# Kernel tuning notes

Hardware: AMD Instinct MI355X
Metric: run time of the kernel (lower is better)

## Reference

```python
import jax, jax.numpy as jnp
import numpy as np

IN_DIM, OUT_DIM, HIDDEN = 64, 64, 128


def _cell(x, h, c, w_ih, w_hh, b_ih, b_hh):
    # PyTorch LSTM gate order: i, f, g, o
    gates = x @ w_ih.T + b_ih + h @ w_hh.T + b_hh
    i, f, g, o = jnp.split(gates, 4, axis=-1)
    c = jax.nn.sigmoid(f) * c + jax.nn.sigmoid(i) * jnp.tanh(g)
    h = jax.nn.sigmoid(o) * jnp.tanh(c)
    return h, c


def setup_inputs() -> dict:
    key = jax.random.key(0)
    ks = jax.random.split(key, 12)
    B, S = 8192, 128
    s = 1.0 / np.sqrt(HIDDEN)
    u = lambda k, shp: jax.random.uniform(k, shp, jnp.float32, -s, s)
    return {
        "x": jax.random.normal(ks[0], (B, S, IN_DIM), jnp.float32),
        "w_ih0": u(ks[1], (4 * HIDDEN, IN_DIM)),
        "w_hh0": u(ks[2], (4 * HIDDEN, HIDDEN)),
        "b_ih0": u(ks[3], (4 * HIDDEN,)),
        "b_hh0": u(ks[4], (4 * HIDDEN,)),
        "w_ih1": u(ks[5], (4 * HIDDEN, HIDDEN)),
        "w_hh1": u(ks[6], (4 * HIDDEN, HIDDEN)),
        "b_ih1": u(ks[7], (4 * HIDDEN,)),
        "b_hh1": u(ks[8], (4 * HIDDEN,)),
        "w_dec": u(ks[9], (OUT_DIM, HIDDEN)),
        "b_dec": u(ks[10], (OUT_DIM,)),
        "pred_steps": 20,
    }


def reference(x, w_ih0, w_hh0, b_ih0, b_hh0, w_ih1, w_hh1, b_ih1, b_hh1, w_dec, b_dec, pred_steps):
    B = x.shape[0]
    z = jnp.zeros((B, HIDDEN), x.dtype)

    def enc_step(carry, xt):
        h0, c0, h1, c1 = carry
        h0, c0 = _cell(xt, h0, c0, w_ih0, w_hh0, b_ih0, b_hh0)
        h1, c1 = _cell(h0, h1, c1, w_ih1, w_hh1, b_ih1, b_hh1)
        return (h0, c0, h1, c1), None

    carry, _ = jax.lax.scan(enc_step, (z, z, z, z), jnp.swapaxes(x, 0, 1))

    def dec_step(carry, _):
        inp, h0, c0, h1, c1 = carry
        h0, c0 = _cell(inp, h0, c0, w_ih0, w_hh0, b_ih0, b_hh0)
        h1, c1 = _cell(h0, h1, c1, w_ih1, w_hh1, b_ih1, b_hh1)
        p = h1 @ w_dec.T + b_dec
        return (p, h0, c0, h1, c1), p

    _, preds = jax.lax.scan(dec_step, (x[:, -1, :],) + carry, None, length=pred_steps)
    return jnp.swapaxes(preds, 0, 1)  # [B, pred_steps, out_dim]
```

## Files before the change

kernel.cpp:

```cpp
#include <hip/hip_runtime.h>
#include <cstdint>
#include <cstddef>

#define BATCH  8192
#define INDIM  64
#define OUTDIM 64
#define HID    128
#define BT     32
#define NT     512
#define KP     328
#define COLH0  64
#define COLH1  192
#define KB0    6
#define KB1    8
#define KBD    4

#define W0U    0
#define W1U    196608
#define WDU    458752
#define B0F    237568
#define B1F    238080
#define BDF    238592
#define NPACK  238656

typedef unsigned short u16;
typedef __attribute__((ext_vector_type(8))) short bfrag;
typedef __attribute__((ext_vector_type(4))) float facc;

__device__ __forceinline__ u16 f2bf(float x) {
  uint32_t u = __float_as_uint(x);
  return (u16)((u + 0x7fffu + ((u >> 16) & 1u)) >> 16);
}
__device__ __forceinline__ float bf2f(u16 h) {
  return __uint_as_float(((uint32_t)h) << 16);
}
__device__ __forceinline__ float fsig(float x) { return 1.0f / (1.0f + __expf(-x)); }
__device__ __forceinline__ float ftanh(float x) {
  float e = __expf(2.0f * x);
  return 1.0f - 2.0f / (e + 1.0f);
}
__device__ __forceinline__ facc splat4(float v) {
  facc a; a[0] = v; a[1] = v; a[2] = v; a[3] = v; return a;
}

template <int KB>
__device__ __forceinline__ void gemm_block(const u16* __restrict__ wt,
                                           const u16 (&Hhi)[BT][KP],
                                           const u16 (&Hlo)[BT][KP],
                                           int colOff, int c, int g, int ntq,
                                           facc (&acc)[2][4]) {
#pragma unroll
  for (int kb = 0; kb < KB; ++kb) {
    bfrag bh[4], bl[4], ah[2], al[2];
#pragma unroll
    for (int t = 0; t < 4; ++t) {
      const u16* p = wt + (((ntq + t) * KB + kb) * 2) * 512;
      bh[t] = *(const bfrag*)p;
      bl[t] = *(const bfrag*)(p + 512);
    }
    const int k0 = colOff + kb * 32 + g * 8;
#pragma unroll
    for (int mt = 0; mt < 2; ++mt) {
      ah[mt] = *(const bfrag*)&Hhi[mt * 16 + c][k0];
      al[mt] = *(const bfrag*)&Hlo[mt * 16 + c][k0];
    }
#pragma unroll
    for (int mt = 0; mt < 2; ++mt)
#pragma unroll
      for (int t = 0; t < 4; ++t) {
        facc a = acc[mt][t];
        a = __builtin_amdgcn_mfma_f32_16x16x32_bf16(ah[mt], bh[t], a, 0, 0, 0);
        a = __builtin_amdgcn_mfma_f32_16x16x32_bf16(ah[mt], bl[t], a, 0, 0, 0);
        a = __builtin_amdgcn_mfma_f32_16x16x32_bf16(al[mt], bh[t], a, 0, 0, 0);
        acc[mt][t] = a;
      }
  }
}

__global__ __launch_bounds__(NT, 2) void lstm_kernel(
    const float* __restrict__ x, const void* __restrict__ pkv,
    float* __restrict__ out, int S, int P) {
  __shared__ __align__(16) u16 Ahi[BT][KP];
  __shared__ __align__(16) u16 Alo[BT][KP];

  const u16* pku = (const u16*)pkv;
  const float* pkf = (const float*)pkv;

  const int tid = threadIdx.x;
  const int lane = tid & 63;
  const int w = tid >> 6;
  const int c = lane & 15;
  const int g = lane >> 4;
  const int b0 = blockIdx.x * BT;

  for (int i = tid; i < BT * KP; i += NT) {
    (&Ahi[0][0])[i] = 0;
    (&Alo[0][0])[i] = 0;
  }

  float b0r[4], b1r[4];
#pragma unroll
  for (int t = 0; t < 4; ++t) {
    b0r[t] = pkf[B0F + (w * 4 + t) * 16 + c];
    b1r[t] = pkf[B1F + (w * 4 + t) * 16 + c];
  }
  const int ntd = w & 3, mtd = w >> 2;
  const float bdr = pkf[BDF + ntd * 16 + c];

  float c0r[8], c1r[8];
#pragma unroll
  for (int q = 0; q < 8; ++q) { c0r[q] = 0.f; c1r[q] = 0.f; }

  const u16* w0t = pku + W0U + lane * 8;
  const u16* w1t = pku + W1U + lane * 8;
  const u16* wdt = pku + WDU + lane * 8;

  __syncthreads();

  const int T = S + P;
  for (int step = 0; step < T; ++step) {
    if (step < S) {
      const int s = tid >> 4, c4 = (tid & 15) * 4;
      const float4 v = *(const float4*)(x + ((size_t)(b0 + s) * S + step) * INDIM + c4);
      float vv[4] = {v.x, v.y, v.z, v.w};
      u16 h4[4], l4[4];
#pragma unroll
      for (int q = 0; q < 4; ++q) {
        h4[q] = f2bf(vv[q]);
        l4[q] = f2bf(vv[q] - bf2f(h4[q]));
      }
      uint2 hp, lp;
      hp.x = (uint32_t)h4[0] | ((uint32_t)h4[1] << 16);
      hp.y = (uint32_t)h4[2] | ((uint32_t)h4[3] << 16);
      lp.x = (uint32_t)l4[0] | ((uint32_t)l4[1] << 16);
      lp.y = (uint32_t)l4[2] | ((uint32_t)l4[3] << 16);
      *(uint2*)&Ahi[s][c4] = hp;
      *(uint2*)&Alo[s][c4] = lp;
    }
    __syncthreads();

    facc acc[2][4];
#pragma unroll
    for (int mt = 0; mt < 2; ++mt)
#pragma unroll
      for (int t = 0; t < 4; ++t) acc[mt][t] = splat4(b0r[t]);
    gemm_block<KB0>(w0t, Ahi, Alo, 0, c, g, w * 4, acc);
    __syncthreads();
#pragma unroll
    for (int mt = 0; mt < 2; ++mt)
#pragma unroll
      for (int r = 0; r < 4; ++r) {
        float gi = fsig(acc[mt][0][r]);
        float gf = fsig(acc[mt][1][r]);
        float gg = ftanh(acc[mt][2][r]);
        float go = fsig(acc[mt][3][r]);
        float cn = fmaf(gf, c0r[mt * 4 + r], gi * gg);
        c0r[mt * 4 + r] = cn;
        float hv = go * ftanh(cn);
        const int s = mt * 16 + g * 4 + r;
        u16 hh = f2bf(hv);
        Ahi[s][COLH0 + w * 16 + c] = hh;
        Alo[s][COLH0 + w * 16 + c] = f2bf(hv - bf2f(hh));
      }
    __syncthreads();

#pragma unroll
    for (int mt = 0; mt < 2; ++mt)
#pragma unroll
      for (int t = 0; t < 4; ++t) acc[mt][t] = splat4(b1r[t]);
    gemm_block<KB1>(w1t, Ahi, Alo, COLH0, c, g, w * 4, acc);
    __syncthreads();
#pragma unroll
    for (int mt = 0; mt < 2; ++mt)
#pragma unroll
      for (int r = 0; r < 4; ++r) {
        float gi = fsig(acc[mt][0][r]);
        float gf = fsig(acc[mt][1][r]);
        float gg = ftanh(acc[mt][2][r]);
        float go = fsig(acc[mt][3][r]);
        float cn = fmaf(gf, c1r[mt * 4 + r], gi * gg);
        c1r[mt * 4 + r] = cn;
        float hv = go * ftanh(cn);
        const int s = mt * 16 + g * 4 + r;
        u16 hh = f2bf(hv);
        Ahi[s][COLH1 + w * 16 + c] = hh;
        Alo[s][COLH1 + w * 16 + c] = f2bf(hv - bf2f(hh));
      }

    if (step >= S) {
      __syncthreads();
      facc da = splat4(bdr);
#pragma unroll
      for (int kb = 0; kb < KBD; ++kb) {
        const u16* p = wdt + ((ntd * KBD + kb) * 2) * 512;
        bfrag wbh = *(const bfrag*)p;
        bfrag wbl = *(const bfrag*)(p + 512);
        const int k0 = COLH1 + kb * 32 + g * 8;
        bfrag dah = *(const bfrag*)&Ahi[mtd * 16 + c][k0];
        bfrag dal = *(const bfrag*)&Alo[mtd * 16 + c][k0];
        da = __builtin_amdgcn_mfma_f32_16x16x32_bf16(dah, wbh, da, 0, 0, 0);
        da = __builtin_amdgcn_mfma_f32_16x16x32_bf16(dah, wbl, da, 0, 0, 0);
        da = __builtin_amdgcn_mfma_f32_16x16x32_bf16(dal, wbh, da, 0, 0, 0);
      }
      const int dstep = step - S;
#pragma unroll
      for (int r = 0; r < 4; ++r) {
        const int s = mtd * 16 + g * 4 + r;
        const int o = ntd * 16 + c;
        float pv = da[r];
        out[((size_t)(b0 + s) * P + dstep) * OUTDIM + o] = pv;
        u16 hh = f2bf(pv);
        Ahi[s][o] = hh;
        Alo[s][o] = f2bf(pv - bf2f(hh));
      }
    }
  }
}

__global__ void prepack_kernel(const float* __restrict__ wih0, const float* __restrict__ whh0,
                               const float* __restrict__ bih0, const float* __restrict__ bhh0,
                               const float* __restrict__ wih1, const float* __restrict__ whh1,
                               const float* __restrict__ bih1, const float* __restrict__ bhh1,
                               const float* __restrict__ wdec, const float* __restrict__ bdec,
                               void* __restrict__ pko) {
  int idx = blockIdx.x * blockDim.x + threadIdx.x;
  if (idx >= NPACK) return;
  u16* pu = (u16*)pko;
  float* pf = (float*)pko;
  if (idx < 98304) {
    int nt = idx / 3072, rem = idx % 3072;
    int kb = rem >> 9, q = rem & 511, ln = q >> 3, j = q & 7;
    int n = nt * 16 + (ln & 15);
    int row = ((n >> 4) & 3) * HID + (n >> 6) * 16 + (n & 15);
    int k = kb * 32 + (ln >> 4) * 8 + j;
    float wv = (k < INDIM) ? wih0[row * INDIM + k] : whh0[row * HID + k - INDIM];
    u16 hi = f2bf(wv), lo = f2bf(wv - bf2f(hi));
    int base = W0U + ((nt * KB0 + kb) * 2) * 512;
    pu[base + q] = hi;
    pu[base + 512 + q] = lo;
  } else if (idx < 229376) {
    int r = idx - 98304;
    int nt = r >> 12, rem = r & 4095;
    int kb = rem >> 9, q = rem & 511, ln = q >> 3, j = q & 7;
    int n = nt * 16 + (ln & 15);
    int row = ((n >> 4) & 3) * HID + (n >> 6) * 16 + (n & 15);
    int k = kb * 32 + (ln >> 4) * 8 + j;
    float wv = (k < HID) ? wih1[row * HID + k] : whh1[row * HID + k - HID];
    u16 hi = f2bf(wv), lo = f2bf(wv - bf2f(hi));
    int base = W1U + ((nt * KB1 + kb) * 2) * 512;
    pu[base + q] = hi;
    pu[base + 512 + q] = lo;
  } else if (idx < 237568) {
    int r = idx - 229376;
    int nt = r >> 11, rem = r & 2047;
    int kb = rem >> 9, q = rem & 511, ln = q >> 3, j = q & 7;
    int o = nt * 16 + (ln & 15);
    int k = kb * 32 + (ln >> 4) * 8 + j;
    float wv = wdec[o * HID + k];
    u16 hi = f2bf(wv), lo = f2bf(wv - bf2f(hi));
    int base = WDU + ((nt * KBD + kb) * 2) * 512;
    pu[base + q] = hi;
    pu[base + 512 + q] = lo;
  } else if (idx < 238080) {
    int n = idx - 237568;
    int row = ((n >> 4) & 3) * HID + (n >> 6) * 16 + (n & 15);
    pf[B0F + n] = bih0[row] + bhh0[row];
  } else if (idx < 238592) {
    int n = idx - 238080;
    int row = ((n >> 4) & 3) * HID + (n >> 6) * 16 + (n & 15);
    pf[B1F + n] = bih1[row] + bhh1[row];
  } else {
    int o = idx - 238592;
    pf[BDF + o] = bdec[o];
  }
}

extern "C" void kernel_launch(void* const* d_in, const int* in_sizes, int n_in,
                              void* d_out, int out_size, void* d_ws, size_t ws_size,
                              hipStream_t stream) {
  const float* x    = (const float*)d_in[0];
  const float* wih0 = (const float*)d_in[1];
  const float* whh0 = (const float*)d_in[2];
  const float* bih0 = (const float*)d_in[3];
  const float* bhh0 = (const float*)d_in[4];
  const float* wih1 = (const float*)d_in[5];
  const float* whh1 = (const float*)d_in[6];
  const float* bih1 = (const float*)d_in[7];
  const float* bhh1 = (const float*)d_in[8];
  const float* wdec = (const float*)d_in[9];
  const float* bdec = (const float*)d_in[10];
  float* out = (float*)d_out;

  const int S = in_sizes[0] / (BATCH * INDIM);
  const int P = out_size / (BATCH * OUTDIM);

  prepack_kernel<<<(NPACK + 255) / 256, 256, 0, stream>>>(
      wih0, whh0, bih0, bhh0, wih1, whh1, bih1, bhh1, wdec, bdec, d_ws);

  lstm_kernel<<<BATCH / BT, NT, 0, stream>>>(x, d_ws, out, S, P);
}
```

Measured before the change: 4.720 ms.

## Double batch tile to 64 rows and prefetch weight fragments across k-blocks

Each block now handles 64 batch rows instead of 32, so every weight fragment read from global memory feeds twice as many MFMAs, and the grid shrinks to half as many blocks. The GEMM loop also double-buffers weight fragments, loading the next k-block while the current one is in use. The cost is roughly double LDS (about 84 KB per block) and many more accumulator and cell-state registers, which will likely drop occupancy below the two blocks per CU that launch_bounds requests. The prefetch buffers add further register pressure and risk spills.

```diff
diff --git a/kernel.cpp b/kernel.cpp
--- a/kernel.cpp
+++ b/kernel.cpp
@@ -6,7 +6,7 @@
 #define INDIM  64
 #define OUTDIM 64
 #define HID    128
-#define BT     32
+#define BT     64
 #define NT     512
 #define KP     328
 #define COLH0  64
@@ -48,30 +48,41 @@
                                            const u16 (&Hhi)[BT][KP],
                                            const u16 (&Hlo)[BT][KP],
                                            int colOff, int c, int g, int ntq,
-                                           facc (&acc)[2][4]) {
+                                           facc (&acc)[4][4]) {
+  bfrag wa[8], wb[8];
+#pragma unroll
+  for (int t = 0; t < 4; ++t) {
+    const u16* p = wt + (((ntq + t) * KB + 0) * 2) * 512;
+    wa[t * 2]     = *(const bfrag*)p;
+    wa[t * 2 + 1] = *(const bfrag*)(p + 512);
+  }
 #pragma unroll
   for (int kb = 0; kb < KB; ++kb) {
-    bfrag bh[4], bl[4], ah[2], al[2];
-#pragma unroll
-    for (int t = 0; t < 4; ++t) {
-      const u16* p = wt + (((ntq + t) * KB + kb) * 2) * 512;
-      bh[t] = *(const bfrag*)p;
-      bl[t] = *(const bfrag*)(p + 512);
+    bfrag (&cur)[8] = (kb & 1) ? wb : wa;
+    bfrag (&nxt)[8] = (kb & 1) ? wa : wb;
+    if (kb + 1 < KB) {
+#pragma unroll
+      for (int t = 0; t < 4; ++t) {
+        const u16* p = wt + (((ntq + t) * KB + kb + 1) * 2) * 512;
+        nxt[t * 2]     = *(const bfrag*)p;
+        nxt[t * 2 + 1] = *(const bfrag*)(p + 512);
+      }
     }
     const int k0 = colOff + kb * 32 + g * 8;
-#pragma unroll
-    for (int mt = 0; mt < 2; ++mt) {
+    bfrag ah[4], al[4];
+#pragma unroll
+    for (int mt = 0; mt < 4; ++mt) {
       ah[mt] = *(const bfrag*)&Hhi[mt * 16 + c][k0];
       al[mt] = *(const bfrag*)&Hlo[mt * 16 + c][k0];
     }
 #pragma unroll
-    for (int mt = 0; mt < 2; ++mt)
+    for (int mt = 0; mt < 4; ++mt)
 #pragma unroll
       for (int t = 0; t < 4; ++t) {
         facc a = acc[mt][t];
-        a = __builtin_amdgcn_mfma_f32_16x16x32_bf16(ah[mt], bh[t], a, 0, 0, 0);
-        a = __builtin_amdgcn_mfma_f32_16x16x32_bf16(ah[mt], bl[t], a, 0, 0, 0);
-        a = __builtin_amdgcn_mfma_f32_16x16x32_bf16(al[mt], bh[t], a, 0, 0, 0);
+        a = __builtin_amdgcn_mfma_f32_16x16x32_bf16(ah[mt], cur[t * 2],     a, 0, 0, 0);
+        a = __builtin_amdgcn_mfma_f32_16x16x32_bf16(ah[mt], cur[t * 2 + 1], a, 0, 0, 0);
+        a = __builtin_amdgcn_mfma_f32_16x16x32_bf16(al[mt], cur[t * 2],     a, 0, 0, 0);
         acc[mt][t] = a;
       }
   }
@@ -107,9 +118,9 @@
   const int ntd = w & 3, mtd = w >> 2;
   const float bdr = pkf[BDF + ntd * 16 + c];
 
-  float c0r[8], c1r[8];
-#pragma unroll
-  for (int q = 0; q < 8; ++q) { c0r[q] = 0.f; c1r[q] = 0.f; }
+  float c0r[16], c1r[16];
+#pragma unroll
+  for (int q = 0; q < 16; ++q) { c0r[q] = 0.f; c1r[q] = 0.f; }
 
   const u16* w0t = pku + W0U + lane * 8;
   const u16* w1t = pku + W1U + lane * 8;
@@ -120,34 +131,38 @@
   const int T = S + P;
   for (int step = 0; step < T; ++step) {
     if (step < S) {
-      const int s = tid >> 4, c4 = (tid & 15) * 4;
-      const float4 v = *(const float4*)(x + ((size_t)(b0 + s) * S + step) * INDIM + c4);
-      float vv[4] = {v.x, v.y, v.z, v.w};
-      u16 h4[4], l4[4];
-#pragma unroll
-      for (int q = 0; q < 4; ++q) {
-        h4[q] = f2bf(vv[q]);
-        l4[q] = f2bf(vv[q] - bf2f(h4[q]));
-      }
-      uint2 hp, lp;
-      hp.x = (uint32_t)h4[0] | ((uint32_t)h4[1] << 16);
-      hp.y = (uint32_t)h4[2] | ((uint32_t)h4[3] << 16);
-      lp.x = (uint32_t)l4[0] | ((uint32_t)l4[1] << 16);
-      lp.y = (uint32_t)l4[2] | ((uint32_t)l4[3] << 16);
-      *(uint2*)&Ahi[s][c4] = hp;
-      *(uint2*)&Alo[s][c4] = lp;
+#pragma unroll
+      for (int i = 0; i < 2; ++i) {
+        const int q = tid + NT * i;
+        const int s = q >> 4, c4 = (q & 15) * 4;
+        const float4 v = *(const float4*)(x + ((size_t)(b0 + s) * S + step) * INDIM + c4);
+        float vv[4] = {v.x, v.y, v.z, v.w};
+        u16 h4[4], l4[4];
+#pragma unroll
+        for (int qq = 0; qq < 4; ++qq) {
+          h4[qq] = f2bf(vv[qq]);
+          l4[qq] = f2bf(vv[qq] - bf2f(h4[qq]));
+        }
+        uint2 hp, lp;
+        hp.x = (uint32_t)h4[0] | ((uint32_t)h4[1] << 16);
+        hp.y = (uint32_t)h4[2] | ((uint32_t)h4[3] << 16);
+        lp.x = (uint32_t)l4[0] | ((uint32_t)l4[1] << 16);
+        lp.y = (uint32_t)l4[2] | ((uint32_t)l4[3] << 16);
+        *(uint2*)&Ahi[s][c4] = hp;
+        *(uint2*)&Alo[s][c4] = lp;
+      }
     }
     __syncthreads();
 
-    facc acc[2][4];
-#pragma unroll
-    for (int mt = 0; mt < 2; ++mt)
+    facc acc[4][4];
+#pragma unroll
+    for (int mt = 0; mt < 4; ++mt)
 #pragma unroll
       for (int t = 0; t < 4; ++t) acc[mt][t] = splat4(b0r[t]);
     gemm_block<KB0>(w0t, Ahi, Alo, 0, c, g, w * 4, acc);
     __syncthreads();
 #pragma unroll
-    for (int mt = 0; mt < 2; ++mt)
+    for (int mt = 0; mt < 4; ++mt)
 #pragma unroll
       for (int r = 0; r < 4; ++r) {
         float gi = fsig(acc[mt][0][r]);
@@ -165,13 +180,13 @@
     __syncthreads();
 
 #pragma unroll
-    for (int mt = 0; mt < 2; ++mt)
+    for (int mt = 0; mt < 4; ++mt)
 #pragma unroll
       for (int t = 0; t < 4; ++t) acc[mt][t] = splat4(b1r[t]);
     gemm_block<KB1>(w1t, Ahi, Alo, COLH0, c, g, w * 4, acc);
     __syncthreads();
 #pragma unroll
-    for (int mt = 0; mt < 2; ++mt)
+    for (int mt = 0; mt < 4; ++mt)
 #pragma unroll
       for (int r = 0; r < 4; ++r) {
         float gi = fsig(acc[mt][0][r]);
@@ -189,29 +204,37 @@
 
     if (step >= S) {
       __syncthreads();
-      facc da = splat4(bdr);
+      facc da[2] = {splat4(bdr), splat4(bdr)};
 #pragma unroll
       for (int kb = 0; kb < KBD; ++kb) {
         const u16* p = wdt + ((ntd * KBD + kb) * 2) * 512;
         bfrag wbh = *(const bfrag*)p;
         bfrag wbl = *(const bfrag*)(p + 512);
         const int k0 = COLH1 + kb * 32 + g * 8;
-        bfrag dah = *(const bfrag*)&Ahi[mtd * 16 + c][k0];
-        bfrag dal = *(const bfrag*)&Alo[mtd * 16 + c][k0];
-        da = __builtin_amdgcn_mfma_f32_16x16x32_bf16(dah, wbh, da, 0, 0, 0);
-        da = __builtin_amdgcn_mfma_f32_16x16x32_bf16(dah, wbl, da, 0, 0, 0);
-        da = __builtin_amdgcn_mfma_f32_16x16x32_bf16(dal, wbh, da, 0, 0, 0);
+#pragma unroll
+        for (int mi = 0; mi < 2; ++mi) {
+          const int mt = mtd + mi * 2;
+          bfrag dah = *(const bfrag*)&Ahi[mt * 16 + c][k0];
+          bfrag dal = *(const bfrag*)&Alo[mt * 16 + c][k0];
+          da[mi] = __builtin_amdgcn_mfma_f32_16x16x32_bf16(dah, wbh, da[mi], 0, 0, 0);
+          da[mi] = __builtin_amdgcn_mfma_f32_16x16x32_bf16(dah, wbl, da[mi], 0, 0, 0);
+          da[mi] = __builtin_amdgcn_mfma_f32_16x16x32_bf16(dal, wbh, da[mi], 0, 0, 0);
+        }
       }
       const int dstep = step - S;
 #pragma unroll
-      for (int r = 0; r < 4; ++r) {
-        const int s = mtd * 16 + g * 4 + r;
-        const int o = ntd * 16 + c;
-        float pv = da[r];
-        out[((size_t)(b0 + s) * P + dstep) * OUTDIM + o] = pv;
-        u16 hh = f2bf(pv);
-        Ahi[s][o] = hh;
-        Alo[s][o] = f2bf(pv - bf2f(hh));
+      for (int mi = 0; mi < 2; ++mi) {
+        const int mt = mtd + mi * 2;
+#pragma unroll
+        for (int r = 0; r < 4; ++r) {
+          const int s = mt * 16 + g * 4 + r;
+          const int o = ntd * 16 + c;
+          float pv = da[mi][r];
+          out[((size_t)(b0 + s) * P + dstep) * OUTDIM + o] = pv;
+          u16 hh = f2bf(pv);
+          Ahi[s][o] = hh;
+          Alo[s][o] = f2bf(pv - bf2f(hh));
+        }
       }
     }
   }
```

New measurement: 5.508 ms. 1.17x slower.

## Double-buffer hidden state, split M across 16 waves, prefetch x, trim barriers

Applied to the files above, without the earlier changes.

Moves the block to 1024 threads, with each wave handling half the batch rows instead of both M tiles. It double-buffers the h0/h1 columns in LDS by step parity, which removes the write-after-read barriers between the GEMM and the activation phases. The next timestep's x is prefetched into registers and written during the layer-0 epilogue. Lighter lgkmcnt-only barriers and s_setprio around the MFMA bursts are added. The cost is one block per CU with a larger LDS footprint, and each wave now reloads the full weight fragments while doing half the M work, which doubles weight traffic per step.

```diff
diff --git a/kernel.cpp b/kernel.cpp
--- a/kernel.cpp
+++ b/kernel.cpp
@@ -7,13 +7,14 @@
 #define OUTDIM 64
 #define HID    128
 #define BT     32
-#define NT     512
-#define KP     328
-#define COLH0  64
-#define COLH1  192
+#define NT     1024
+#define KP2    584
 #define KB0    6
 #define KB1    8
 #define KBD    4
+
+#define XH0(p) (64 + 128 * (p))
+#define XH1(p) (320 + 128 * (p))
 
 #define W0U    0
 #define W1U    196608
@@ -43,45 +44,51 @@
   facc a; a[0] = v; a[1] = v; a[2] = v; a[3] = v; return a;
 }
 
-template <int KB>
-__device__ __forceinline__ void gemm_block(const u16* __restrict__ wt,
-                                           const u16 (&Hhi)[BT][KP],
-                                           const u16 (&Hlo)[BT][KP],
-                                           int colOff, int c, int g, int ntq,
-                                           facc (&acc)[2][4]) {
+__device__ __forceinline__ void bar_lds() {
+  __builtin_amdgcn_sched_barrier(0);
+  asm volatile("s_waitcnt lgkmcnt(0)" ::: "memory");
+  __builtin_amdgcn_s_barrier();
+  __builtin_amdgcn_sched_barrier(0);
+}
+
+template <int KB, int SPLIT>
+__device__ __forceinline__ void gemm_run(const u16* __restrict__ wt,
+                                         const u16 (&Hhi)[BT][KP2],
+                                         const u16 (&Hlo)[BT][KP2],
+                                         int off1, int off2,
+                                         int c, int g, int mh, int ntq,
+                                         facc (&acc)[4]) {
 #pragma unroll
   for (int kb = 0; kb < KB; ++kb) {
-    bfrag bh[4], bl[4], ah[2], al[2];
-#pragma unroll
-    for (int t = 0; t < 4; ++t) {
-      const u16* p = wt + (((ntq + t) * KB + kb) * 2) * 512;
-      bh[t] = *(const bfrag*)p;
-      bl[t] = *(const bfrag*)(p + 512);
-    }
-    const int k0 = colOff + kb * 32 + g * 8;
-#pragma unroll
-    for (int mt = 0; mt < 2; ++mt) {
-      ah[mt] = *(const bfrag*)&Hhi[mt * 16 + c][k0];
-      al[mt] = *(const bfrag*)&Hlo[mt * 16 + c][k0];
-    }
-#pragma unroll
-    for (int mt = 0; mt < 2; ++mt)
-#pragma unroll
-      for (int t = 0; t < 4; ++t) {
-        facc a = acc[mt][t];
-        a = __builtin_amdgcn_mfma_f32_16x16x32_bf16(ah[mt], bh[t], a, 0, 0, 0);
-        a = __builtin_amdgcn_mfma_f32_16x16x32_bf16(ah[mt], bl[t], a, 0, 0, 0);
-        a = __builtin_amdgcn_mfma_f32_16x16x32_bf16(al[mt], bh[t], a, 0, 0, 0);
-        acc[mt][t] = a;
-      }
-  }
-}
-
-__global__ __launch_bounds__(NT, 2) void lstm_kernel(
+    bfrag wf[8];
+#pragma unroll
+    for (int tt = 0; tt < 4; ++tt) {
+      const u16* p = wt + (((ntq + tt) * KB + kb) * 2) * 512;
+      wf[tt * 2]     = *(const bfrag*)p;
+      wf[tt * 2 + 1] = *(const bfrag*)(p + 512);
+    }
+    const int colA = ((kb < SPLIT) ? off1 + kb * 32
+                                   : off2 + (kb - SPLIT) * 32) + g * 8;
+    const bfrag ah = *(const bfrag*)&Hhi[mh * 16 + c][colA];
+    const bfrag al = *(const bfrag*)&Hlo[mh * 16 + c][colA];
+    __builtin_amdgcn_s_setprio(1);
+#pragma unroll
+    for (int tt = 0; tt < 4; ++tt) {
+      facc a = acc[tt];
+      a = __builtin_amdgcn_mfma_f32_16x16x32_bf16(ah, wf[tt * 2],     a, 0, 0, 0);
+      a = __builtin_amdgcn_mfma_f32_16x16x32_bf16(ah, wf[tt * 2 + 1], a, 0, 0, 0);
+      a = __builtin_amdgcn_mfma_f32_16x16x32_bf16(al, wf[tt * 2],     a, 0, 0, 0);
+      acc[tt] = a;
+    }
+    __builtin_amdgcn_s_setprio(0);
+  }
+}
+
+__global__ __launch_bounds__(NT, 1) void lstm_kernel(
     const float* __restrict__ x, const void* __restrict__ pkv,
     float* __restrict__ out, int S, int P) {
-  __shared__ __align__(16) u16 Ahi[BT][KP];
-  __shared__ __align__(16) u16 Alo[BT][KP];
+  __shared__ __align__(16) u16 Ahi[BT][KP2];
+  __shared__ __align__(16) u16 Alo[BT][KP2];
 
   const u16* pku = (const u16*)pkv;
   const float* pkf = (const float*)pkv;
@@ -89,11 +96,15 @@
   const int tid = threadIdx.x;
   const int lane = tid & 63;
   const int w = tid >> 6;
+  const int wq = w & 7;
+  const int mh = w >> 3;
   const int c = lane & 15;
   const int g = lane >> 4;
+  const int ntq = wq * 4;
   const int b0 = blockIdx.x * BT;
-
-  for (int i = tid; i < BT * KP; i += NT) {
+  const int jcol = wq * 16 + c;
+
+  for (int i = tid; i < BT * KP2; i += NT) {
     (&Ahi[0][0])[i] = 0;
     (&Alo[0][0])[i] = 0;
   }
@@ -101,119 +112,136 @@
   float b0r[4], b1r[4];
 #pragma unroll
   for (int t = 0; t < 4; ++t) {
-    b0r[t] = pkf[B0F + (w * 4 + t) * 16 + c];
-    b1r[t] = pkf[B1F + (w * 4 + t) * 16 + c];
-  }
-  const int ntd = w & 3, mtd = w >> 2;
+    b0r[t] = pkf[B0F + (ntq + t) * 16 + c];
+    b1r[t] = pkf[B1F + (ntq + t) * 16 + c];
+  }
+  const int ntd = w & 3, mtd = (w >> 2) & 1;
   const float bdr = pkf[BDF + ntd * 16 + c];
 
-  float c0r[8], c1r[8];
-#pragma unroll
-  for (int q = 0; q < 8; ++q) { c0r[q] = 0.f; c1r[q] = 0.f; }
+  float c0r[4], c1r[4];
+#pragma unroll
+  for (int q = 0; q < 4; ++q) { c0r[q] = 0.f; c1r[q] = 0.f; }
 
   const u16* w0t = pku + W0U + lane * 8;
   const u16* w1t = pku + W1U + lane * 8;
   const u16* wdt = pku + WDU + lane * 8;
 
-  __syncthreads();
-
+  const int sx = tid >> 4, cx = (tid & 15) * 4;
+  float4 xr = make_float4(0.f, 0.f, 0.f, 0.f);
+  if (tid < 512) {
+    const float4 v = *(const float4*)(x + (size_t)(b0 + sx) * S * INDIM + cx);
+    float vv[4] = {v.x, v.y, v.z, v.w};
+#pragma unroll
+    for (int q = 0; q < 4; ++q) {
+      u16 hh = f2bf(vv[q]);
+      Ahi[sx][cx + q] = hh;
+      Alo[sx][cx + q] = f2bf(vv[q] - bf2f(hh));
+    }
+    if (S > 1) xr = *(const float4*)(x + ((size_t)(b0 + sx) * S + 1) * INDIM + cx);
+  }
+
+  bar_lds();
+
+  int par = 0;
   const int T = S + P;
   for (int step = 0; step < T; ++step) {
-    if (step < S) {
-      const int s = tid >> 4, c4 = (tid & 15) * 4;
-      const float4 v = *(const float4*)(x + ((size_t)(b0 + s) * S + step) * INDIM + c4);
-      float vv[4] = {v.x, v.y, v.z, v.w};
-      u16 h4[4], l4[4];
-#pragma unroll
-      for (int q = 0; q < 4; ++q) {
-        h4[q] = f2bf(vv[q]);
-        l4[q] = f2bf(vv[q] - bf2f(h4[q]));
-      }
-      uint2 hp, lp;
-      hp.x = (uint32_t)h4[0] | ((uint32_t)h4[1] << 16);
-      hp.y = (uint32_t)h4[2] | ((uint32_t)h4[3] << 16);
-      lp.x = (uint32_t)l4[0] | ((uint32_t)l4[1] << 16);
-      lp.y = (uint32_t)l4[2] | ((uint32_t)l4[3] << 16);
-      *(uint2*)&Ahi[s][c4] = hp;
-      *(uint2*)&Alo[s][c4] = lp;
-    }
-    __syncthreads();
-
-    facc acc[2][4];
-#pragma unroll
-    for (int mt = 0; mt < 2; ++mt)
-#pragma unroll
-      for (int t = 0; t < 4; ++t) acc[mt][t] = splat4(b0r[t]);
-    gemm_block<KB0>(w0t, Ahi, Alo, 0, c, g, w * 4, acc);
-    __syncthreads();
-#pragma unroll
-    for (int mt = 0; mt < 2; ++mt)
+    facc acc[4];
+#pragma unroll
+    for (int t = 0; t < 4; ++t) acc[t] = splat4(b0r[t]);
+    gemm_run<KB0, 2>(w0t, Ahi, Alo, 0, XH0(par), c, g, mh, ntq, acc);
+    bar_lds();
+
+    {
+      const int col0 = XH0(par ^ 1) + jcol;
 #pragma unroll
       for (int r = 0; r < 4; ++r) {
-        float gi = fsig(acc[mt][0][r]);
-        float gf = fsig(acc[mt][1][r]);
-        float gg = ftanh(acc[mt][2][r]);
-        float go = fsig(acc[mt][3][r]);
-        float cn = fmaf(gf, c0r[mt * 4 + r], gi * gg);
-        c0r[mt * 4 + r] = cn;
+        float gi = fsig(acc[0][r]);
+        float gf = fsig(acc[1][r]);
+        float gg = ftanh(acc[2][r]);
+        float go = fsig(acc[3][r]);
+        float cn = fmaf(gf, c0r[r], gi * gg);
+        c0r[r] = cn;
         float hv = go * ftanh(cn);
-        const int s = mt * 16 + g * 4 + r;
+        const int s = mh * 16 + g * 4 + r;
         u16 hh = f2bf(hv);
-        Ahi[s][COLH0 + w * 16 + c] = hh;
-        Alo[s][COLH0 + w * 16 + c] = f2bf(hv - bf2f(hh));
-      }
-    __syncthreads();
-
-#pragma unroll
-    for (int mt = 0; mt < 2; ++mt)
-#pragma unroll
-      for (int t = 0; t < 4; ++t) acc[mt][t] = splat4(b1r[t]);
-    gemm_block<KB1>(w1t, Ahi, Alo, COLH0, c, g, w * 4, acc);
-    __syncthreads();
-#pragma unroll
-    for (int mt = 0; mt < 2; ++mt)
+        Ahi[s][col0] = hh;
+        Alo[s][col0] = f2bf(hv - bf2f(hh));
+      }
+    }
+    if (tid < 512) {
+      if (step + 1 < S) {
+        float vv[4] = {xr.x, xr.y, xr.z, xr.w};
+#pragma unroll
+        for (int q = 0; q < 4; ++q) {
+          u16 hh = f2bf(vv[q]);
+          Ahi[sx][cx + q] = hh;
+          Alo[sx][cx + q] = f2bf(vv[q] - bf2f(hh));
+        }
+      }
+      if (step + 2 < S)
+        xr = *(const float4*)(x + ((size_t)(b0 + sx) * S + step + 2) * INDIM + cx);
+    }
+    bar_lds();
+
+#pragma unroll
+    for (int t = 0; t < 4; ++t) acc[t] = splat4(b1r[t]);
+    gemm_run<KB1, 4>(w1t, Ahi, Alo, XH0(par ^ 1), XH1(par), c, g, mh, ntq, acc);
+
+    {
+      const int col1 = XH1(par ^ 1) + jcol;
 #pragma unroll
       for (int r = 0; r < 4; ++r) {
-        float gi = fsig(acc[mt][0][r]);
-        float gf = fsig(acc[mt][1][r]);
-        float gg = ftanh(acc[mt][2][r]);
-        float go = fsig(acc[mt][3][r]);
-        float cn = fmaf(gf, c1r[mt * 4 + r], gi * gg);
-        c1r[mt * 4 + r] = cn;
+        float gi = fsig(acc[0][r]);
+        float gf = fsig(acc[1][r]);
+        float gg = ftanh(acc[2][r]);
+        float go = fsig(acc[3][r]);
+        float cn = fmaf(gf, c1r[r], gi * gg);
+        c1r[r] = cn;
         float hv = go * ftanh(cn);
-        const int s = mt * 16 + g * 4 + r;
+        const int s = mh * 16 + g * 4 + r;
         u16 hh = f2bf(hv);
-        Ahi[s][COLH1 + w * 16 + c] = hh;
-        Alo[s][COLH1 + w * 16 + c] = f2bf(hv - bf2f(hh));
-      }
+        Ahi[s][col1] = hh;
+        Alo[s][col1] = f2bf(hv - bf2f(hh));
+      }
+    }
 
     if (step >= S) {
-      __syncthreads();
-      facc da = splat4(bdr);
-#pragma unroll
-      for (int kb = 0; kb < KBD; ++kb) {
-        const u16* p = wdt + ((ntd * KBD + kb) * 2) * 512;
-        bfrag wbh = *(const bfrag*)p;
-        bfrag wbl = *(const bfrag*)(p + 512);
-        const int k0 = COLH1 + kb * 32 + g * 8;
-        bfrag dah = *(const bfrag*)&Ahi[mtd * 16 + c][k0];
-        bfrag dal = *(const bfrag*)&Alo[mtd * 16 + c][k0];
-        da = __builtin_amdgcn_mfma_f32_16x16x32_bf16(dah, wbh, da, 0, 0, 0);
-        da = __builtin_amdgcn_mfma_f32_16x16x32_bf16(dah, wbl, da, 0, 0, 0);
-        da = __builtin_amdgcn_mfma_f32_16x16x32_bf16(dal, wbh, da, 0, 0, 0);
-      }
-      const int dstep = step - S;
-#pragma unroll
-      for (int r = 0; r < 4; ++r) {
-        const int s = mtd * 16 + g * 4 + r;
-        const int o = ntd * 16 + c;
-        float pv = da[r];
-        out[((size_t)(b0 + s) * P + dstep) * OUTDIM + o] = pv;
-        u16 hh = f2bf(pv);
-        Ahi[s][o] = hh;
-        Alo[s][o] = f2bf(pv - bf2f(hh));
-      }
-    }
+      bfrag wdf[8];
+      if (w < 8) {
+#pragma unroll
+        for (int kb = 0; kb < KBD; ++kb) {
+          const u16* p = wdt + ((ntd * KBD + kb) * 2) * 512;
+          wdf[kb * 2]     = *(const bfrag*)p;
+          wdf[kb * 2 + 1] = *(const bfrag*)(p + 512);
+        }
+      }
+      bar_lds();
+      if (w < 8) {
+        facc da = splat4(bdr);
+#pragma unroll
+        for (int kb = 0; kb < KBD; ++kb) {
+          const int colA = XH1(par ^ 1) + kb * 32 + g * 8;
+          const bfrag dah = *(const bfrag*)&Ahi[mtd * 16 + c][colA];
+          const bfrag dal = *(const bfrag*)&Alo[mtd * 16 + c][colA];
+          da = __builtin_amdgcn_mfma_f32_16x16x32_bf16(dah, wdf[kb * 2],     da, 0, 0, 0);
+          da = __builtin_amdgcn_mfma_f32_16x16x32_bf16(dah, wdf[kb * 2 + 1], da, 0, 0, 0);
+          da = __builtin_amdgcn_mfma_f32_16x16x32_bf16(dal, wdf[kb * 2],     da, 0, 0, 0);
+        }
+        const int dstep = step - S;
+#pragma unroll
+        for (int r = 0; r < 4; ++r) {
+          const int s = mtd * 16 + g * 4 + r;
+          const int o = ntd * 16 + c;
+          float pv = da[r];
+          out[((size_t)(b0 + s) * P + dstep) * OUTDIM + o] = pv;
+          u16 hh = f2bf(pv);
+          Ahi[s][o] = hh;
+          Alo[s][o] = f2bf(pv - bf2f(hh));
+        }
+      }
+      bar_lds();
+    }
+    par ^= 1;
   }
 }
 
```

New measurement: 11.55 ms. 2.45x slower.
